# Kernel tuning notes

Hardware: AMD Instinct MI355X
Metric: run time of the kernel (lower is better)

The kernel has to match this reference:

```python
import jax, jax.numpy as jnp
import numpy as np

N_IN = 512
N_OUT = 256
T = 2048
B = 32


def setup_inputs() -> dict:
    key = jax.random.key(0)
    ks = jax.random.split(key, 9)
    s_in = 1.0 / np.sqrt(N_IN)
    inp = {
        "xt": jax.random.normal(ks[0], (T, B, N_IN), dtype=jnp.float32),
        "ct_forward": jax.random.normal(ks[1], (1, B, N_OUT), dtype=jnp.float32),
        # weights stored torch-style as [out, in]
        "Wx": jax.random.uniform(ks[2], (N_OUT, N_IN), jnp.float32, -s_in, s_in),
        "Wf": jax.random.uniform(ks[3], (N_OUT, N_IN), jnp.float32, -s_in, s_in),
        "bf": jax.random.uniform(ks[4], (N_OUT,), jnp.float32, -s_in, s_in),
        "Wr": jax.random.uniform(ks[5], (N_OUT, N_IN), jnp.float32, -s_in, s_in),
        "br": jax.random.uniform(ks[6], (N_OUT,), jnp.float32, -s_in, s_in),
        "Wc": jax.random.uniform(ks[7], (N_OUT, N_IN), jnp.float32, -s_in, s_in),
        "bc": jax.random.uniform(ks[8], (N_OUT,), jnp.float32, -s_in, s_in),
    }
    return inp


def reference(xt, ct_forward, Wx, Wf, bf, Wr, br, Wc, bc):
    # Batched projections over all timesteps (the GEMM part of SRU).
    x_proj = jnp.einsum("tbi,oi->tbo", xt, Wx)              # [T,B,n_out]
    f = jax.nn.sigmoid(jnp.einsum("tbi,oi->tbo", xt, Wf) + bf)
    r = jax.nn.sigmoid(jnp.einsum("tbi,oi->tbo", xt, Wr) + br)
    cx = jnp.einsum("tbi,oi->tbo", xt, Wc) + bc

    def step(c, inp):
        x_t, ft, rt, cxt = inp
        c = ft * c + (1.0 - ft) * x_t
        h = rt * jnp.tanh(c) + (1.0 - rt) * cxt
        return c, h

    c_final, ht = jax.lax.scan(step, ct_forward[0], (x_proj, f, r, cx))
    # dropout=0.0 -> identity; forward returns (ht, ct)
    return ht, c_final
```

## Files before the change

### kernel.cpp

```cpp
#include <hip/hip_runtime.h>
#include <stdint.h>

#define T_STEPS 2048
#define BATCH   32
#define NIN     512
#define NOUT    256
#define MROWS   (T_STEPS*BATCH)
#define BO      (BATCH*NOUT)
#define NCHUNK  32
#define CHLEN   (T_STEPS/NCHUNK)

typedef _Float16 f16x8 __attribute__((ext_vector_type(8)));
typedef _Float16 f16x4 __attribute__((ext_vector_type(4)));
typedef float    fx4   __attribute__((ext_vector_type(4)));

#define LDSP(p) ((__attribute__((address_space(3))) void*)(p))
#define GLBP(p) ((const __attribute__((address_space(1))) void*)(p))

__global__ __launch_bounds__(256) void convert_x(
    const float* __restrict__ xt, _Float16* __restrict__ xh)
{
    long i = ((long)blockIdx.x * 256 + threadIdx.x) * 8;
    float4 v0 = *(const float4*)(xt + i);
    float4 v1 = *(const float4*)(xt + i + 4);
    f16x8 h;
    h[0] = (_Float16)v0.x; h[1] = (_Float16)v0.y;
    h[2] = (_Float16)v0.z; h[3] = (_Float16)v0.w;
    h[4] = (_Float16)v1.x; h[5] = (_Float16)v1.y;
    h[6] = (_Float16)v1.z; h[7] = (_Float16)v1.w;
    *(f16x8*)(xh + i) = h;
}

__global__ __launch_bounds__(256) void convert_w(
    const float* __restrict__ Wx, const float* __restrict__ Wf,
    const float* __restrict__ Wr, const float* __restrict__ Wc,
    _Float16* __restrict__ Wcat)
{
    int idx = blockIdx.x * 256 + threadIdx.x;
    int n  = idx >> 7;
    int k4 = (idx & 127) * 4;
    int g = n >> 8, o = n & 255;
    const float* W = (g == 0) ? Wx : (g == 1) ? Wf : (g == 2) ? Wr : Wc;
    float4 v = *(const float4*)(W + o * NIN + k4);
    f16x4 h;
    h[0] = (_Float16)v.x; h[1] = (_Float16)v.y;
    h[2] = (_Float16)v.z; h[3] = (_Float16)v.w;
    *(f16x4*)(Wcat + n * NIN + k4) = h;
}

#define BM 128
#define BN 128
#define BK 64

__global__ __launch_bounds__(256) void gemm_proj(
    const _Float16* __restrict__ xh,
    const _Float16* __restrict__ Wcat,
    const float* __restrict__ bfv, const float* __restrict__ brv, const float* __restrict__ bcv,
    _Float16* __restrict__ xp_h, _Float16* __restrict__ f_h,
    _Float16* __restrict__ r_h,  _Float16* __restrict__ cx_h)
{
    __shared__ _Float16 As[BM * BK];
    __shared__ _Float16 Bs[BN * BK];
    char* AsB = (char*)As;
    char* BsB = (char*)Bs;

    const int tid  = threadIdx.x;
    const int lane = tid & 63;
    const int w    = tid >> 6;
    const int wr = w >> 1, wc = w & 1;
    const int lr = lane & 15, lk = lane >> 4;

    int wg = (blockIdx.x & 7) * 512 + (blockIdx.x >> 3);
    const int  rowblk = wg >> 3;
    const int  cg     = wg & 7;
    const long m0 = (long)rowblk * BM;
    const int  n0 = cg * BN;

    const int src_cl = (((lane & 7) ^ (lane >> 3)) << 4);
    const char* gA = (const char*)xh +
        (m0 + w * 32 + (lane >> 3)) * (NIN * 2) + src_cl;
    const char* gB = (const char*)Wcat +
        ((long)n0 + w * 32 + (lane >> 3)) * (NIN * 2) + src_cl;
    char* ldsA = AsB + w * 4096;
    char* ldsB = BsB + w * 4096;

    fx4 acc[4][4];
    #pragma unroll
    for (int i = 0; i < 4; ++i)
        #pragma unroll
        for (int j = 0; j < 4; ++j) acc[i][j] = (fx4){0.f, 0.f, 0.f, 0.f};

    for (int kb = 0; kb < NIN / BK; ++kb) {
        #pragma unroll
        for (int it = 0; it < 4; ++it)
            __builtin_amdgcn_global_load_lds(GLBP(gA + it * (8 * NIN * 2) + kb * (BK * 2)),
                                             LDSP(ldsA + it * 1024), 16, 0, 0);
        #pragma unroll
        for (int it = 0; it < 4; ++it)
            __builtin_amdgcn_global_load_lds(GLBP(gB + it * (8 * NIN * 2) + kb * (BK * 2)),
                                             LDSP(ldsB + it * 1024), 16, 0, 0);
        __syncthreads();

        #pragma unroll
        for (int kk = 0; kk < 2; ++kk) {
            f16x8 af[4], bg[4];
            const int kbyte = kk * 64 + lk * 16;
            #pragma unroll
            for (int mf = 0; mf < 4; ++mf) {
                int row = wr * 64 + mf * 16 + lr;
                af[mf] = *(const f16x8*)(AsB + row * 128 + (kbyte ^ ((row & 7) << 4)));
            }
            #pragma unroll
            for (int nf = 0; nf < 4; ++nf) {
                int row = wc * 64 + nf * 16 + lr;
                bg[nf] = *(const f16x8*)(BsB + row * 128 + (kbyte ^ ((row & 7) << 4)));
            }
            #pragma unroll
            for (int mf = 0; mf < 4; ++mf)
                #pragma unroll
                for (int nf = 0; nf < 4; ++nf)
                    acc[mf][nf] = __builtin_amdgcn_mfma_f32_16x16x32_f16(
                        af[mf], bg[nf], acc[mf][nf], 0, 0, 0);
        }
        __syncthreads();
    }

    const int g = cg >> 1;
    const int obase = (cg & 1) * 128;
    _Float16* outp = (g == 0) ? xp_h : (g == 1) ? f_h : (g == 2) ? r_h : cx_h;
    const float* bias = (g == 1) ? bfv : (g == 2) ? brv : (g == 3) ? bcv : nullptr;
    #pragma unroll
    for (int mf = 0; mf < 4; ++mf) {
        #pragma unroll
        for (int nf = 0; nf < 4; ++nf) {
            int o = obase + wc * 64 + nf * 16 + lr;
            float bv = (g == 0) ? 0.f : bias[o];
            #pragma unroll
            for (int j = 0; j < 4; ++j) {
                long row = m0 + wr * 64 + mf * 16 + lk * 4 + j;
                float v = acc[mf][nf][j] + bv;
                _Float16 hv;
                if (g == 1 || g == 2) {
                    float e = __expf(-v);
                    hv = (_Float16)(__builtin_amdgcn_rcpf(1.0f + e));
                } else {
                    hv = (_Float16)v;
                }
                outp[row * NOUT + o] = hv;
            }
        }
    }
}

__global__ __launch_bounds__(256) void chunk_scan_a(
    const _Float16* __restrict__ f_h, const _Float16* __restrict__ xp_h,
    float* __restrict__ chunkA, float* __restrict__ chunkB)
{
    int tid = blockIdx.x * 256 + threadIdx.x;
    int chunk = tid >> 13;
    int bo = tid & (BO - 1);
    long base = (long)chunk * CHLEN * BO + bo;
    float a = 1.f, cc = 0.f;
    #pragma unroll 4
    for (int s = 0; s < CHLEN; ++s) {
        long i = base + (long)s * BO;
        float fv = (float)f_h[i];
        float xv = (float)xp_h[i];
        cc = fv * cc + (1.f - fv) * xv;
        a *= fv;
    }
    chunkA[tid] = a;
    chunkB[tid] = cc;
}

__global__ __launch_bounds__(256) void chunk_prop(
    const float* __restrict__ ct0,
    const float* __restrict__ chunkA, const float* __restrict__ chunkB,
    float* __restrict__ cin, float* __restrict__ c_final)
{
    int bo = blockIdx.x * 256 + threadIdx.x;
    float c = ct0[bo];
    #pragma unroll
    for (int ch = 0; ch < NCHUNK; ++ch) {
        cin[ch * BO + bo] = c;
        c = chunkA[ch * BO + bo] * c + chunkB[ch * BO + bo];
    }
    c_final[bo] = c;
}

__global__ __launch_bounds__(256) void chunk_scan_h(
    const _Float16* __restrict__ xp_h, const _Float16* __restrict__ f_h,
    const _Float16* __restrict__ r_h,  const _Float16* __restrict__ cx_h,
    const float* __restrict__ cin, float* __restrict__ ht)
{
    int tid = blockIdx.x * 256 + threadIdx.x;
    int chunk = tid >> 13;
    int bo = tid & (BO - 1);
    long base = (long)chunk * CHLEN * BO + bo;
    float c = cin[tid];
    #pragma unroll 4
    for (int s = 0; s < CHLEN; ++s) {
        long i = base + (long)s * BO;
        float fv = (float)f_h[i];
        float xv = (float)xp_h[i];
        float rv = (float)r_h[i];
        float cxv = (float)cx_h[i];
        c = fv * c + (1.f - fv) * xv;
        float e = __expf(2.f * c);
        float th = (e - 1.f) * __builtin_amdgcn_rcpf(e + 1.f);
        ht[i] = rv * th + (1.f - rv) * cxv;
    }
}

extern "C" void kernel_launch(void* const* d_in, const int* in_sizes, int n_in,
                              void* d_out, int out_size, void* d_ws, size_t ws_size,
                              hipStream_t stream) {
    const float* xt  = (const float*)d_in[0];
    const float* ct0 = (const float*)d_in[1];
    const float* Wx  = (const float*)d_in[2];
    const float* Wf  = (const float*)d_in[3];
    const float* bf_ = (const float*)d_in[4];
    const float* Wr  = (const float*)d_in[5];
    const float* br_ = (const float*)d_in[6];
    const float* Wc  = (const float*)d_in[7];
    const float* bc_ = (const float*)d_in[8];

    float* ht      = (float*)d_out;
    float* c_final = ht + (size_t)MROWS * NOUT;

    char* ws = (char*)d_ws;
    _Float16* Wcat = (_Float16*)ws;
    _Float16* xh   = (_Float16*)(ws + (1 << 20));
    _Float16* xp_h = xh + (size_t)MROWS * NIN;
    _Float16* f_h  = xp_h + (size_t)MROWS * NOUT;
    _Float16* r_h  = f_h  + (size_t)MROWS * NOUT;
    _Float16* cx_h = r_h  + (size_t)MROWS * NOUT;
    float* chunkA  = (float*)(cx_h + (size_t)MROWS * NOUT);
    float* chunkB  = chunkA + NCHUNK * BO;
    float* cin     = chunkB + NCHUNK * BO;

    convert_w<<<512, 256, 0, stream>>>(Wx, Wf, Wr, Wc, Wcat);
    convert_x<<<(MROWS * NIN / 8) / 256, 256, 0, stream>>>(xt, xh);
    gemm_proj<<<(MROWS / BM) * 8, 256, 0, stream>>>(
        xh, Wcat, bf_, br_, bc_, xp_h, f_h, r_h, cx_h);
    chunk_scan_a<<<(NCHUNK * BO) / 256, 256, 0, stream>>>(f_h, xp_h, chunkA, chunkB);
    chunk_prop<<<BO / 256, 256, 0, stream>>>(ct0, chunkA, chunkB, cin, c_final);
    chunk_scan_h<<<(NCHUNK * BO) / 256, 256, 0, stream>>>(xp_h, f_h, r_h, cx_h, cin, ht);
}
```

Baseline: 206.0 us.

## Rewrite projection GEMM as 256x256 tile with double-buffered pipelined LDS loads

The projection GEMM moves from 128x128 tiles with 256 threads to 256x256 tiles with 512 threads. K-tiles are double-buffered in 128KB of LDS, and async global-to-LDS loads for later half-tiles are interleaved with MFMA quadrants, using explicit barriers, waitcnt and setprio. This aims to raise data reuse per tile and hide global load latency that the old single-buffered load-sync-compute loop exposed. The cost is more LDS, which limits occupancy to one block per CU, and a fragile hand-written synchronisation schedule.

```diff
diff --git a/kernel.cpp b/kernel.cpp
--- a/kernel.cpp
+++ b/kernel.cpp
@@ -16,6 +16,10 @@
 
 #define LDSP(p) ((__attribute__((address_space(3))) void*)(p))
 #define GLBP(p) ((const __attribute__((address_space(1))) void*)(p))
+
+#define BAR()       asm volatile("s_barrier" ::: "memory")
+#define WAITLGKM0() do { asm volatile("s_waitcnt lgkmcnt(0)" ::: "memory"); __builtin_amdgcn_sched_barrier(0); } while(0)
+#define WAITVM(n)   do { asm volatile("s_waitcnt vmcnt(" #n ")" ::: "memory"); __builtin_amdgcn_sched_barrier(0); } while(0)
 
 __global__ __launch_bounds__(256) void convert_x(
     const float* __restrict__ xt, _Float16* __restrict__ xh)
@@ -48,105 +52,162 @@
     *(f16x4*)(Wcat + n * NIN + k4) = h;
 }
 
-#define BM 128
-#define BN 128
+#define BM 256
+#define BN 256
 #define BK 64
-
-__global__ __launch_bounds__(256) void gemm_proj(
+#define NKT (NIN / BK)
+
+__global__ __launch_bounds__(512) void gemm_proj(
     const _Float16* __restrict__ xh,
     const _Float16* __restrict__ Wcat,
     const float* __restrict__ bfv, const float* __restrict__ brv, const float* __restrict__ bcv,
     _Float16* __restrict__ xp_h, _Float16* __restrict__ f_h,
     _Float16* __restrict__ r_h,  _Float16* __restrict__ cx_h)
 {
-    __shared__ _Float16 As[BM * BK];
-    __shared__ _Float16 Bs[BN * BK];
-    char* AsB = (char*)As;
-    char* BsB = (char*)Bs;
+    __shared__ char lds[131072];
 
     const int tid  = threadIdx.x;
     const int lane = tid & 63;
     const int w    = tid >> 6;
-    const int wr = w >> 1, wc = w & 1;
+    const int wrq  = w >> 2;
+    const int wcq  = w & 3;
     const int lr = lane & 15, lk = lane >> 4;
 
-    int wg = (blockIdx.x & 7) * 512 + (blockIdx.x >> 3);
-    const int  rowblk = wg >> 3;
-    const int  cg     = wg & 7;
+    int wg = (blockIdx.x & 7) * 128 + (blockIdx.x >> 3);
+    const int  rowblk = wg >> 2;
+    const int  cg     = wg & 3;
     const long m0 = (long)rowblk * BM;
     const int  n0 = cg * BN;
 
-    const int src_cl = (((lane & 7) ^ (lane >> 3)) << 4);
-    const char* gA = (const char*)xh +
-        (m0 + w * 32 + (lane >> 3)) * (NIN * 2) + src_cl;
-    const char* gB = (const char*)Wcat +
-        ((long)n0 + w * 32 + (lane >> 3)) * (NIN * 2) + src_cl;
-    char* ldsA = AsB + w * 4096;
-    char* ldsB = BsB + w * 4096;
-
-    fx4 acc[4][4];
+    const int rl8  = lane >> 3;
+    const int scol = (((lane & 7) ^ rl8) << 4);
+    const char* baseA = (const char*)xh   + (m0 + w * 8 + rl8) * 1024 + scol;
+    const char* baseB = (const char*)Wcat + ((long)(n0 + w * 8 + rl8)) * 1024 + scol;
+
+#define STAGE_A(t, h) do {                                                   \
+        char* _d = lds + ((t) & 1) * 32768 + (h) * 16384 + w * 1024;         \
+        const char* _s = baseA + (long)(h) * 131072 + (t) * 128;             \
+        __builtin_amdgcn_global_load_lds(GLBP(_s),         LDSP(_d),        16, 0, 0); \
+        __builtin_amdgcn_global_load_lds(GLBP(_s + 65536), LDSP(_d + 8192), 16, 0, 0); \
+    } while (0)
+#define STAGE_B(t, h) do {                                                   \
+        char* _d = lds + 65536 + ((t) & 1) * 32768 + (h) * 16384 + w * 1024; \
+        const char* _s = baseB + (long)(h) * 131072 + (t) * 128;             \
+        __builtin_amdgcn_global_load_lds(GLBP(_s),         LDSP(_d),        16, 0, 0); \
+        __builtin_amdgcn_global_load_lds(GLBP(_s + 65536), LDSP(_d + 8192), 16, 0, 0); \
+    } while (0)
+
+    fx4 acc[2][2][4][2];
     #pragma unroll
-    for (int i = 0; i < 4; ++i)
+    for (int a = 0; a < 2; ++a)
         #pragma unroll
-        for (int j = 0; j < 4; ++j) acc[i][j] = (fx4){0.f, 0.f, 0.f, 0.f};
-
-    for (int kb = 0; kb < NIN / BK; ++kb) {
-        #pragma unroll
-        for (int it = 0; it < 4; ++it)
-            __builtin_amdgcn_global_load_lds(GLBP(gA + it * (8 * NIN * 2) + kb * (BK * 2)),
-                                             LDSP(ldsA + it * 1024), 16, 0, 0);
-        #pragma unroll
-        for (int it = 0; it < 4; ++it)
-            __builtin_amdgcn_global_load_lds(GLBP(gB + it * (8 * NIN * 2) + kb * (BK * 2)),
-                                             LDSP(ldsB + it * 1024), 16, 0, 0);
-        __syncthreads();
-
-        #pragma unroll
-        for (int kk = 0; kk < 2; ++kk) {
-            f16x8 af[4], bg[4];
-            const int kbyte = kk * 64 + lk * 16;
+        for (int b = 0; b < 2; ++b)
             #pragma unroll
-            for (int mf = 0; mf < 4; ++mf) {
-                int row = wr * 64 + mf * 16 + lr;
-                af[mf] = *(const f16x8*)(AsB + row * 128 + (kbyte ^ ((row & 7) << 4)));
-            }
-            #pragma unroll
-            for (int nf = 0; nf < 4; ++nf) {
-                int row = wc * 64 + nf * 16 + lr;
-                bg[nf] = *(const f16x8*)(BsB + row * 128 + (kbyte ^ ((row & 7) << 4)));
-            }
-            #pragma unroll
-            for (int mf = 0; mf < 4; ++mf)
+            for (int c = 0; c < 4; ++c)
                 #pragma unroll
-                for (int nf = 0; nf < 4; ++nf)
-                    acc[mf][nf] = __builtin_amdgcn_mfma_f32_16x16x32_f16(
-                        af[mf], bg[nf], acc[mf][nf], 0, 0, 0);
-        }
-        __syncthreads();
-    }
-
-    const int g = cg >> 1;
-    const int obase = (cg & 1) * 128;
+                for (int d = 0; d < 2; ++d)
+                    acc[a][b][c][d] = (fx4){0.f, 0.f, 0.f, 0.f};
+
+    f16x8 Ar[4][2];
+    f16x8 B0r[2][2];
+    f16x8 B1r[2][2];
+
+#define READ_A(c2, h) do {                                                   \
+        _Pragma("unroll")                                                    \
+        for (int mf = 0; mf < 4; ++mf) {                                     \
+            int rl = wrq * 64 + mf * 16 + lr;                                \
+            int rb = (c2) * 32768 + (h) * 16384 + rl * 128;                  \
+            _Pragma("unroll")                                                \
+            for (int kk = 0; kk < 2; ++kk)                                   \
+                Ar[mf][kk] = *(const f16x8*)(lds + rb +                      \
+                    ((kk * 64 + lk * 16) ^ ((rl & 7) << 4)));                \
+        }                                                                    \
+    } while (0)
+#define READ_B(c2, h, dst) do {                                              \
+        _Pragma("unroll")                                                    \
+        for (int nf = 0; nf < 2; ++nf) {                                     \
+            int rl = wcq * 32 + nf * 16 + lr;                                \
+            int rb = 65536 + (c2) * 32768 + (h) * 16384 + rl * 128;          \
+            _Pragma("unroll")                                                \
+            for (int kk = 0; kk < 2; ++kk)                                   \
+                dst[nf][kk] = *(const f16x8*)(lds + rb +                     \
+                    ((kk * 64 + lk * 16) ^ ((rl & 7) << 4)));                \
+        }                                                                    \
+    } while (0)
+#define MMACC(Qr, Qc, Br) do {                                               \
+        __builtin_amdgcn_s_setprio(1);                                       \
+        _Pragma("unroll")                                                    \
+        for (int kk = 0; kk < 2; ++kk)                                       \
+            _Pragma("unroll")                                                \
+            for (int mf = 0; mf < 4; ++mf)                                   \
+                _Pragma("unroll")                                            \
+                for (int nf = 0; nf < 2; ++nf)                               \
+                    acc[Qr][Qc][mf][nf] = __builtin_amdgcn_mfma_f32_16x16x32_f16( \
+                        Ar[mf][kk], Br[nf][kk], acc[Qr][Qc][mf][nf], 0, 0, 0);    \
+        __builtin_amdgcn_s_setprio(0);                                       \
+    } while (0)
+
+    STAGE_A(0, 0); STAGE_B(0, 0); STAGE_B(0, 1); STAGE_A(0, 1);
+    STAGE_A(1, 0); STAGE_B(1, 0);
+    WAITVM(4);
+    BAR();
+
+    for (int t = 0; t < NKT; ++t) {
+        const int c2 = t & 1;
+        READ_A(c2, 0);
+        READ_B(c2, 0, B0r);
+        if (t + 1 < NKT) STAGE_B(t + 1, 1);
+        BAR();
+        WAITLGKM0();
+        MMACC(0, 0, B0r);
+        BAR();
+        READ_B(c2, 1, B1r);
+        if (t + 1 < NKT) STAGE_A(t + 1, 1);
+        BAR();
+        WAITLGKM0();
+        MMACC(0, 1, B1r);
+        BAR();
+        READ_A(c2, 1);
+        if (t + 2 < NKT) STAGE_A(t + 2, 0);
+        BAR();
+        WAITLGKM0();
+        MMACC(1, 0, B0r);
+        BAR();
+        if (t + 2 < NKT) STAGE_B(t + 2, 0);
+        BAR();
+        MMACC(1, 1, B1r);
+        if (t < NKT - 2)       WAITVM(4);
+        else if (t == NKT - 2) WAITVM(0);
+        BAR();
+    }
+
+    const int g = cg;
     _Float16* outp = (g == 0) ? xp_h : (g == 1) ? f_h : (g == 2) ? r_h : cx_h;
     const float* bias = (g == 1) ? bfv : (g == 2) ? brv : (g == 3) ? bcv : nullptr;
     #pragma unroll
-    for (int mf = 0; mf < 4; ++mf) {
+    for (int Qr = 0; Qr < 2; ++Qr) {
         #pragma unroll
-        for (int nf = 0; nf < 4; ++nf) {
-            int o = obase + wc * 64 + nf * 16 + lr;
-            float bv = (g == 0) ? 0.f : bias[o];
+        for (int Qc = 0; Qc < 2; ++Qc) {
             #pragma unroll
-            for (int j = 0; j < 4; ++j) {
-                long row = m0 + wr * 64 + mf * 16 + lk * 4 + j;
-                float v = acc[mf][nf][j] + bv;
-                _Float16 hv;
-                if (g == 1 || g == 2) {
-                    float e = __expf(-v);
-                    hv = (_Float16)(__builtin_amdgcn_rcpf(1.0f + e));
-                } else {
-                    hv = (_Float16)v;
+            for (int mf = 0; mf < 4; ++mf) {
+                #pragma unroll
+                for (int nf = 0; nf < 2; ++nf) {
+                    int o = Qc * 128 + wcq * 32 + nf * 16 + lr;
+                    float bv = (g == 0) ? 0.f : bias[o];
+                    #pragma unroll
+                    for (int j = 0; j < 4; ++j) {
+                        long row = m0 + Qr * 128 + wrq * 64 + mf * 16 + lk * 4 + j;
+                        float v = acc[Qr][Qc][mf][nf][j] + bv;
+                        _Float16 hv;
+                        if (g == 1 || g == 2) {
+                            float e = __expf(-v);
+                            hv = (_Float16)(__builtin_amdgcn_rcpf(1.0f + e));
+                        } else {
+                            hv = (_Float16)v;
+                        }
+                        outp[row * NOUT + o] = hv;
+                    }
                 }
-                outp[row * NOUT + o] = hv;
             }
         }
     }
@@ -241,7 +302,7 @@
 
     convert_w<<<512, 256, 0, stream>>>(Wx, Wf, Wr, Wc, Wcat);
     convert_x<<<(MROWS * NIN / 8) / 256, 256, 0, stream>>>(xt, xh);
-    gemm_proj<<<(MROWS / BM) * 8, 256, 0, stream>>>(
+    gemm_proj<<<(MROWS / BM) * 4, 512, 0, stream>>>(
         xh, Wcat, bf_, br_, bc_, xp_h, f_h, r_h, cx_h);
     chunk_scan_a<<<(NCHUNK * BO) / 256, 256, 0, stream>>>(f_h, xp_h, chunkA, chunkB);
     chunk_prop<<<BO / 256, 256, 0, stream>>>(ct0, chunkA, chunkB, cin, c_final);
```

Result: faster. 194.5 us (-5.6%).
